# Kernel tuning notes

Hardware: AMD Instinct MI355X
Metric: run time of the kernel (lower is better)

## Reference

```python
import jax, jax.numpy as jnp
from jax import lax
import numpy as np

# Geometry derived from module.calibrate() for input [2,64,768,768], k=3, s=1, bcount=(16,16)
N, CIN, COUT, H, W = 2, 64, 64, 768, 768
K, STRIDE = 3, 1
BC = 16            # block count per spatial dim
PAD = 1            # total pad 2 -> 1 each side (H and W)
BSIZE = 50         # gathered block size (input space, padded input is 770)
BOUT = 48          # conv output size per block
BSTR = 48          # block stride (= bsize - k + stride); also scatter stride
NBLK = 256
BN_EPS = 1e-3


def setup_inputs() -> dict:
    key = jax.random.key(0)
    ks = jax.random.split(key, 7)
    x = jax.random.normal(ks[0], (N, CIN, H, W), jnp.float32)
    conv_w = jax.random.normal(ks[1], (COUT, CIN, K, K), jnp.float32) * 0.05
    conv_b = jax.random.normal(ks[2], (COUT,), jnp.float32) * 0.1
    gamma = jax.random.uniform(ks[3], (COUT,), jnp.float32, 0.5, 1.5)
    beta = jax.random.normal(ks[4], (COUT,), jnp.float32) * 0.1
    run_mean = jax.random.normal(ks[5], (COUT,), jnp.float32) * 0.1
    run_var = jax.random.uniform(ks[6], (COUT,), jnp.float32, 0.5, 1.5)
    # unique active blocks (n, bh, bw) as in ReduceMask.active_block_indices
    rng = np.random.default_rng(0)
    all_blocks = np.stack(np.meshgrid(np.arange(N), np.arange(BC), np.arange(BC),
                                      indexing='ij'), axis=-1).reshape(-1, 3)
    sel = rng.permutation(all_blocks.shape[0])[:NBLK]
    abi = jnp.asarray(all_blocks[sel], jnp.int32)
    return dict(x=x, conv_w=conv_w, conv_b=conv_b, gamma=gamma, beta=beta,
                run_mean=run_mean, run_var=run_var, active_block_indices=abi)


def reference(x, conv_w, conv_b, gamma, beta, run_mean, run_var, active_block_indices):
    # pad as in F.pad(padding_params)
    xp = jnp.pad(x, ((0, 0), (0, 0), (PAD, PAD), (PAD, PAD)))  # [N,C,770,770]
    nidx = active_block_indices[:, 0]                          # [B]
    hh = active_block_indices[:, 1][:, None] * BSTR + jnp.arange(BSIZE)[None, :]  # [B,50]
    ww = active_block_indices[:, 2][:, None] * BSTR + jnp.arange(BSIZE)[None, :]  # [B,50]
    # sparse_gather: extract [B,50,50,C] blocks (vectorized advanced indexing)
    xp_nhwc = xp.transpose(0, 2, 3, 1)
    p = xp_nhwc[nidx[:, None, None], hh[:, :, None], ww[:, None, :]]   # [B,50,50,C]
    p = p.transpose(0, 3, 1, 2)                                        # [B,C,50,50]
    # conv2d (VALID) + bias
    q = lax.conv_general_dilated(p, conv_w, (STRIDE, STRIDE), 'VALID')
    q = q + conv_b[None, :, None, None]                                # [B,COUT,48,48]
    # BatchNorm (inference: running stats) + ReLU
    inv = gamma / jnp.sqrt(run_var + BN_EPS)
    q = q * inv[None, :, None, None] + (beta - run_mean * inv)[None, :, None, None]
    q = jax.nn.relu(q)
    # sparse_scatter (add=False) into [N,COUT,768,768]; blocks are non-overlapping
    ho = active_block_indices[:, 1][:, None] * BSTR + jnp.arange(BOUT)[None, :]
    wo = active_block_indices[:, 2][:, None] * BSTR + jnp.arange(BOUT)[None, :]
    y = jnp.zeros((N, H, W, COUT), x.dtype)
    y = y.at[nidx[:, None, None], ho[:, :, None], wo[:, None, :]].set(q.transpose(0, 2, 3, 1))
    return y.transpose(0, 3, 1, 2)
```

## Files before the change

kernel.cpp:

```cpp
#include <hip/hip_runtime.h>


typedef __attribute__((ext_vector_type(8))) short short8;
typedef __attribute__((ext_vector_type(4))) float floatx4;

#define WS_SCALE 0
#define WS_SHIFT 64
#define WS_FLAGS 128
#define WS_WA    640

#define CONV_WGS 1536
#define ZERO_WGS 4096
#define TOTAL_WGS (CONV_WGS + ZERO_WGS)

__device__ __forceinline__ short f2bf(float f) {
  unsigned u = __builtin_bit_cast(unsigned, f);
  u += 0x7fffu + ((u >> 16) & 1u);
  return (short)(u >> 16);
}

__global__ __launch_bounds__(256) void prep_kernel(
    const float* __restrict__ conv_w,
    const float* __restrict__ conv_b,
    const float* __restrict__ gamma,
    const float* __restrict__ beta,
    const float* __restrict__ run_mean,
    const float* __restrict__ run_var,
    const int* __restrict__ abi,
    float* __restrict__ ws) {
  int tid = threadIdx.x;
  if (blockIdx.x == 0) {
    int* flags = (int*)(ws + WS_FLAGS);
    flags[tid] = 0;
    flags[tid + 256] = 0;
    __syncthreads();
    int n = abi[3 * tid + 0];
    int bh = abi[3 * tid + 1];
    int bw = abi[3 * tid + 2];
    flags[n * 256 + bh * 16 + bw] = 1;
    if (tid < 64) {
      float inv = gamma[tid] * rsqrtf(run_var[tid] + 1e-3f);
      ws[WS_SCALE + tid] = inv;
      ws[WS_SHIFT + tid] = (conv_b[tid] - run_mean[tid]) * inv + beta[tid];
    }
  }
  short* wa = (short*)(ws + WS_WA);
  for (int d = blockIdx.x * 256 + tid; d < 49152; d += 64 * 256) {
    int j = d & 7;
    int q = (d >> 3) & 3;
    int cout = (d >> 5) & 63;
    int ks = d >> 11;
    int kt = ks % 3;
    int cc = ks / 3;
    int tap = kt * 4 + q;
    short v = 0;
    if (tap < 9) {
      int ci = cc * 8 + j;
      int dy = tap / 3;
      int dx = tap - dy * 3;
      v = f2bf(conv_w[((cout * 64 + ci) * 3 + dy) * 3 + dx]);
    }
    wa[d] = v;
  }
}

__global__ __launch_bounds__(512, 4) void main_kernel(
    const float* __restrict__ x,
    const float* __restrict__ ws_f,
    const int* __restrict__ abi,
    float* __restrict__ out) {
  __shared__ __align__(16) short lds[2][4864];

  int braw = blockIdx.x;
  int tid = threadIdx.x;

  int before = (int)(((long long)braw * CONV_WGS) / TOTAL_WGS);
  int after  = (int)(((long long)(braw + 1) * CONV_WGS) / TOTAL_WGS);
  bool is_conv = after > before;

  if (!is_conv) {
    const int* flags = (const int*)(ws_f + WS_FLAGS);
    int z = braw - before;
    int tile = z >> 3;
    int part = z & 7;
    if (flags[tile]) return;
    int n = tile >> 8;
    int bh = (tile >> 4) & 15;
    int bw = tile & 15;
    float* base = out + (((n * 64 + part * 8) * 768 + bh * 48)) * 768 + bw * 48;
    float4 zv = make_float4(0.f, 0.f, 0.f, 0.f);
#pragma unroll
    for (int i = 0; i < 9; ++i) {
      int idx = i * 512 + tid;
      int f = idx % 12;
      int t2 = idx / 12;
      int rr = t2 % 48;
      int c = t2 / 48;
      *((float4*)(base + (c * 768 + rr) * (size_t)768) + f) = zv;
    }
    return;
  }

  int b = before;
  int blk = b / 6;
  int strip = b - blk * 6;
  int n = abi[3 * blk + 0];
  int bh = abi[3 * blk + 1];
  int bw = abi[3 * blk + 2];
  int h0 = bh * 48 + strip * 8;
  int w0 = bw * 48;

  int lane = tid & 63;
  int wv = tid >> 6;
  int ln15 = lane & 15;
  int quad = lane >> 4;

  const float* xn = x + (size_t)n * 64 * 768 * 768;
  const short* wa = (const short*)(ws_f + WS_WA);
  const short* wap = wa + ln15 * 32 + quad * 8;

  if (tid < 8) {
    lds[0][4560 + tid] = 0; lds[0][4704 + tid] = 0; lds[0][4848 + tid] = 0;
    lds[1][4560 + tid] = 0; lds[1][4704 + tid] = 0; lds[1][4848 + tid] = 0;
  }

  int bA[3];
#pragma unroll
  for (int kt = 0; kt < 3; ++kt) {
    int tap = kt * 4 + quad;
    if (tap < 9) {
      int dy = tap / 3;
      int dx = tap - dy * 3;
      int cx = ln15 + dx;
      bA[kt] = ((wv + dy) * 57 + cx + (cx >> 3)) * 16;
    } else {
      bA[kt] = 9120;
    }
  }

  auto load_chunk = [&](int cc8, float4* pf) {
#pragma unroll
    for (int i = 0; i < 3; ++i) {
      int e = i * 512 + tid;
      float4 v = make_float4(0.f, 0.f, 0.f, 0.f);
      if (e < 1120) {
        int f = e % 14;
        int t = e / 14;
        int r = t % 10;
        int ci = t / 10;
        int gh = h0 - 1 + r;
        int gw0 = w0 - 4 + 4 * f;
        if ((unsigned)gh < 768u) {
          const float* rp = xn + ((size_t)(cc8 + ci) * 768 + gh) * 768;
          if (gw0 >= 0 && gw0 <= 764) {
            v = *(const float4*)(rp + gw0);
          } else {
#pragma unroll
            for (int j = 0; j < 4; ++j) {
              int gw = gw0 + j;
              if ((unsigned)gw < 768u) ((float*)&v)[j] = rp[gw];
            }
          }
        }
      }
      pf[i] = v;
    }
  };
  auto store_chunk = [&](int bsel, const float4* pf) {
#pragma unroll
    for (int i = 0; i < 3; ++i) {
      int e = i * 512 + tid;
      if (e < 1120) {
        int f = e % 14;
        int t = e / 14;
        int r = t % 10;
        int ci = t / 10;
        const float* vp = (const float*)&pf[i];
#pragma unroll
        for (int j = 0; j < 4; ++j) {
          int c = 4 * f - 3 + j;
          if ((unsigned)c < 50u) {
            int u = r * 57 + c + (c >> 3);
            lds[bsel][u * 8 + ci] = f2bf(vp[j]);
          }
        }
      }
    }
  };

  float4 pf[3];
  load_chunk(0, pf);
  store_chunk(0, pf);
  __syncthreads();

  floatx4 acc[3][4];
#pragma unroll
  for (int c16 = 0; c16 < 3; ++c16)
#pragma unroll
    for (int mt = 0; mt < 4; ++mt)
      acc[c16][mt] = (floatx4){0.f, 0.f, 0.f, 0.f};

  for (int cc = 0; cc < 8; ++cc) {
    int bsel = cc & 1;
    if (cc < 7) load_chunk((cc + 1) * 8, pf);
    const char* lb = (const char*)lds[bsel];
#pragma unroll
    for (int kt = 0; kt < 3; ++kt) {
      int ks = cc * 3 + kt;
      short8 af[4];
#pragma unroll
      for (int mt = 0; mt < 4; ++mt)
        af[mt] = *(const short8*)(wap + ks * 2048 + mt * 512);
#pragma unroll
      for (int c16 = 0; c16 < 3; ++c16) {
        short8 bf = *(const short8*)(lb + bA[kt] + c16 * 288);
#pragma unroll
        for (int mt = 0; mt < 4; ++mt)
          acc[c16][mt] = __builtin_amdgcn_mfma_f32_16x16x32_bf16(
              af[mt], bf, acc[c16][mt], 0, 0, 0);
      }
    }
    if (cc < 7) store_chunk(bsel ^ 1, pf);
    __syncthreads();
  }

  const float* scale = ws_f + WS_SCALE;
  const float* shift = ws_f + WS_SHIFT;
  float* op = out + (size_t)n * 64 * 768 * 768 + (size_t)(h0 + wv) * 768 + (w0 + ln15);
#pragma unroll
  for (int mt = 0; mt < 4; ++mt) {
#pragma unroll
    for (int reg = 0; reg < 4; ++reg) {
      int cout = mt * 16 + quad * 4 + reg;
      float sc = scale[cout];
      float sh = shift[cout];
#pragma unroll
      for (int c16 = 0; c16 < 3; ++c16) {
        float vv = fmaf(acc[c16][mt][reg], sc, sh);
        vv = vv > 0.f ? vv : 0.f;
        op[(size_t)cout * 589824 + c16 * 16] = vv;
      }
    }
  }
}

extern "C" void kernel_launch(void* const* d_in, const int* in_sizes, int n_in,
                              void* d_out, int out_size, void* d_ws, size_t ws_size,
                              hipStream_t stream) {
  const float* x = (const float*)d_in[0];
  const float* conv_w = (const float*)d_in[1];
  const float* conv_b = (const float*)d_in[2];
  const float* gamma = (const float*)d_in[3];
  const float* beta = (const float*)d_in[4];
  const float* run_mean = (const float*)d_in[5];
  const float* run_var = (const float*)d_in[6];
  const int* abi = (const int*)d_in[7];
  float* out = (float*)d_out;
  float* ws = (float*)d_ws;

  prep_kernel<<<64, 256, 0, stream>>>(conv_w, conv_b, gamma, beta,
                                      run_mean, run_var, abi, ws);
  main_kernel<<<TOTAL_WGS, 512, 0, stream>>>(x, ws, abi, out);
}
```

Measured before the change: 617.1 us.

## Triple-buffer LDS input chunks and place zero-fill blocks after conv blocks

Moves from double to triple buffering of the bf16 input tiles in LDS. Each iteration stores the next chunk and issues the global load for the chunk after it before running the MFMAs, so loads get a full iteration of latency hiding and only one barrier is needed per iteration. It also drops the interleaving of conv and zero-fill workgroups: all conv workgroups now come first and the zero-fill workgroups follow. The extra LDS buffer (about 29 KB per workgroup in total) may lower occupancy, and the new block ordering changes how the two kinds of work are balanced across CUs.

```diff
diff --git a/kernel.cpp b/kernel.cpp
--- a/kernel.cpp
+++ b/kernel.cpp
@@ -11,7 +11,8 @@
 
 #define CONV_WGS 1536
 #define ZERO_WGS 4096
-#define TOTAL_WGS (CONV_WGS + ZERO_WGS)
+
+#define LDS_BUF 4864
 
 __device__ __forceinline__ short f2bf(float f) {
   unsigned u = __builtin_bit_cast(unsigned, f);
@@ -69,18 +70,14 @@
     const float* __restrict__ ws_f,
     const int* __restrict__ abi,
     float* __restrict__ out) {
-  __shared__ __align__(16) short lds[2][4864];
-
-  int braw = blockIdx.x;
+  __shared__ __align__(16) short lds[3 * LDS_BUF];
+
+  int b = blockIdx.x;
   int tid = threadIdx.x;
 
-  int before = (int)(((long long)braw * CONV_WGS) / TOTAL_WGS);
-  int after  = (int)(((long long)(braw + 1) * CONV_WGS) / TOTAL_WGS);
-  bool is_conv = after > before;
-
-  if (!is_conv) {
+  if (b >= CONV_WGS) {
     const int* flags = (const int*)(ws_f + WS_FLAGS);
-    int z = braw - before;
+    int z = b - CONV_WGS;
     int tile = z >> 3;
     int part = z & 7;
     if (flags[tile]) return;
@@ -101,7 +98,6 @@
     return;
   }
 
-  int b = before;
   int blk = b / 6;
   int strip = b - blk * 6;
   int n = abi[3 * blk + 0];
@@ -120,8 +116,12 @@
   const short* wap = wa + ln15 * 32 + quad * 8;
 
   if (tid < 8) {
-    lds[0][4560 + tid] = 0; lds[0][4704 + tid] = 0; lds[0][4848 + tid] = 0;
-    lds[1][4560 + tid] = 0; lds[1][4704 + tid] = 0; lds[1][4848 + tid] = 0;
+#pragma unroll
+    for (int bb = 0; bb < 3; ++bb) {
+      lds[bb * LDS_BUF + 4560 + tid] = 0;
+      lds[bb * LDS_BUF + 4704 + tid] = 0;
+      lds[bb * LDS_BUF + 4848 + tid] = 0;
+    }
   }
 
   int bA[3];
@@ -166,7 +166,7 @@
       pf[i] = v;
     }
   };
-  auto store_chunk = [&](int bsel, const float4* pf) {
+  auto store_chunk = [&](short* dst, const float4* pf) {
 #pragma unroll
     for (int i = 0; i < 3; ++i) {
       int e = i * 512 + tid;
@@ -181,7 +181,7 @@
           int c = 4 * f - 3 + j;
           if ((unsigned)c < 50u) {
             int u = r * 57 + c + (c >> 3);
-            lds[bsel][u * 8 + ci] = f2bf(vp[j]);
+            dst[u * 8 + ci] = f2bf(vp[j]);
           }
         }
       }
@@ -190,8 +190,8 @@
 
   float4 pf[3];
   load_chunk(0, pf);
-  store_chunk(0, pf);
-  __syncthreads();
+  store_chunk(lds, pf);
+  load_chunk(8, pf);
 
   floatx4 acc[3][4];
 #pragma unroll
@@ -200,10 +200,13 @@
     for (int mt = 0; mt < 4; ++mt)
       acc[c16][mt] = (floatx4){0.f, 0.f, 0.f, 0.f};
 
+  int rb = 0;
   for (int cc = 0; cc < 8; ++cc) {
-    int bsel = cc & 1;
-    if (cc < 7) load_chunk((cc + 1) * 8, pf);
-    const char* lb = (const char*)lds[bsel];
+    __syncthreads();
+    int sb = (rb == 2) ? 0 : rb + 1;
+    if (cc < 7) store_chunk(lds + sb * LDS_BUF, pf);
+    if (cc < 6) load_chunk((cc + 2) * 8, pf);
+    const char* lb = (const char*)(lds + rb * LDS_BUF);
 #pragma unroll
     for (int kt = 0; kt < 3; ++kt) {
       int ks = cc * 3 + kt;
@@ -220,8 +223,7 @@
               af[mt], bf, acc[c16][mt], 0, 0, 0);
       }
     }
-    if (cc < 7) store_chunk(bsel ^ 1, pf);
-    __syncthreads();
+    rb = sb;
   }
 
   const float* scale = ws_f + WS_SCALE;
@@ -260,5 +262,5 @@
 
   prep_kernel<<<64, 256, 0, stream>>>(conv_w, conv_b, gamma, beta,
                                       run_mean, run_var, abi, ws);
-  main_kernel<<<TOTAL_WGS, 512, 0, stream>>>(x, ws, abi, out);
-}
+  main_kernel<<<CONV_WGS + ZERO_WGS, 512, 0, stream>>>(x, ws, abi, out);
+}
```

Result: faster. 585.5 us (-5.1%).
